# Performance work log

Hardware: AMD Instinct MI355X
Metric: run time of the kernel (lower is better)

## Reference

```python
import jax, jax.numpy as jnp
import numpy as np

NUM_USERS = 50000
NUM_FOODS = 20000
USER_FEAT_DIM = 256
FOOD_FEAT_DIM = 256
EMBED_DIM = 128
NUM_LAYERS = 3
NUM_HEADS = 4
THRESHOLD = 0.3
E_UF = 600000  # user->food interactions; symmetrized to 2*E_UF directed edges


def setup_inputs() -> dict:
    key = jax.random.key(0)
    ks = jax.random.split(key, 12)
    user_feat = jax.random.normal(ks[0], (NUM_USERS, USER_FEAT_DIM), jnp.float32)
    food_feat = jax.random.normal(ks[1], (NUM_FOODS, FOOD_FEAT_DIM), jnp.float32)
    # bipartite edges in global index space, symmetrized (both directions)
    u = jax.random.randint(ks[2], (E_UF,), 0, NUM_USERS)
    f = jax.random.randint(ks[3], (E_UF,), 0, NUM_FOODS) + NUM_USERS
    edge_index = jnp.stack([jnp.concatenate([u, f]), jnp.concatenate([f, u])]).astype(jnp.int64)
    s = 0.02
    W_user = jax.random.normal(ks[4], (USER_FEAT_DIM, EMBED_DIM), jnp.float32) * s
    b_user = jnp.zeros((EMBED_DIM,), jnp.float32)
    W_food = jax.random.normal(ks[5], (FOOD_FEAT_DIM, EMBED_DIM), jnp.float32) * s
    b_food = jnp.zeros((EMBED_DIM,), jnp.float32)
    Wq = jax.random.normal(ks[6], (EMBED_DIM, EMBED_DIM), jnp.float32) * s
    Wk = jax.random.normal(ks[7], (EMBED_DIM, EMBED_DIM), jnp.float32) * s
    channel_weights = jnp.zeros((2,), jnp.float32)  # StructurePooling fusion weights
    user_embed = jax.random.normal(ks[8], (NUM_USERS, EMBED_DIM), jnp.float32) * 0.1
    item_embed = jax.random.normal(ks[9], (NUM_FOODS, EMBED_DIM), jnp.float32) * 0.1
    return {"user_feat": user_feat, "food_feat": food_feat, "edge_index": edge_index,
            "W_user": W_user, "b_user": b_user, "W_food": W_food, "b_food": b_food,
            "Wq": Wq, "Wk": Wk, "channel_weights": channel_weights,
            "user_embed": user_embed, "item_embed": item_embed}


def reference(user_feat, food_feat, edge_index, W_user, b_user, W_food, b_food,
              Wq, Wk, channel_weights, user_embed, item_embed):
    N = NUM_USERS + NUM_FOODS
    Dh = EMBED_DIM // NUM_HEADS
    # feature projections + relu
    user_emb = jax.nn.relu(user_feat @ W_user + b_user)   # [U, D]
    food_emb = jax.nn.relu(food_feat @ W_food + b_food)   # [F, D]
    row, col = edge_index[0], edge_index[1]
    # graph generator: per-edge multi-head cosine similarity between user/food endpoints
    u_idx = jnp.where(row < NUM_USERS, row, col)
    f_idx = jnp.where(row < NUM_USERS, col, row) - NUM_USERS
    q = (user_emb[u_idx] @ Wq).reshape(-1, NUM_HEADS, Dh)  # [E, H, Dh]
    k = (food_emb[f_idx] @ Wk).reshape(-1, NUM_HEADS, Dh)
    eps = 1e-8
    sim = (q * k).sum(-1) / (jnp.linalg.norm(q, axis=-1) * jnp.linalg.norm(k, axis=-1) + eps)
    mask_feature = (sim.mean(-1) > THRESHOLD).astype(jnp.float32)  # [E]
    # structure pooling fusion of [all-ones, feature mask]
    w = jax.nn.softmax(channel_weights)
    fused = w[0] * 1.0 + w[1] * mask_feature
    edge_mask = (fused > 0.5).astype(jnp.float32)
    # LightGCN: symmetric-normalized propagation on the masked graph
    deg = jnp.maximum(jax.ops.segment_sum(edge_mask, row, num_segments=N), 1.0)
    norm = edge_mask / jnp.sqrt(deg[row] * deg[col])       # [E]
    x0 = jnp.concatenate([user_embed, item_embed], axis=0)  # [N, D]
    x = x0
    acc = x0
    for _ in range(NUM_LAYERS):
        x = jax.ops.segment_sum(norm[:, None] * x[col], row, num_segments=N)
        acc = acc + x
    out = acc / float(NUM_LAYERS + 1)
    return (out[:NUM_USERS], out[NUM_USERS:], user_embed, item_embed)
```

## Files before the change

kernel.cpp:

```cpp
#include <hip/hip_runtime.h>
#include <cstdint>

#define U_NUM 50000
#define F_NUM 20000
#define N_NUM 70000
#define D_EMB 128
#define THRESH 0.3f

typedef _Float16 half8 __attribute__((ext_vector_type(8)));
typedef float f32x4 __attribute__((ext_vector_type(4)));
typedef unsigned short u16x8 __attribute__((ext_vector_type(8)));

__global__ void presplit_zero(const float* __restrict__ Wu, const float* __restrict__ Wf,
                              const float* __restrict__ Wq, const float* __restrict__ Wk,
                              unsigned short* __restrict__ dst,
                              int* __restrict__ cnt, int* __restrict__ cursor)
{
    int i = blockIdx.x * 256 + threadIdx.x;
    if (i < N_NUM) { cnt[i] = 0; cursor[i] = 0; }
    if (i >= 98304) return;
    float a; size_t d; int pstride;
    if (i < 32768) {
        int n = i >> 8, k = i & 255;
        a = Wu[k * 128 + n]; d = (size_t)n * 256 + k; pstride = 32768;
    } else if (i < 65536) {
        int j = i - 32768; int n = j >> 8, k = j & 255;
        a = Wf[k * 128 + n]; d = 65536 + (size_t)n * 256 + k; pstride = 32768;
    } else if (i < 81920) {
        int j = i - 65536; int n = j >> 7, k = j & 127;
        a = Wq[k * 128 + n]; d = 131072 + (size_t)n * 128 + k; pstride = 16384;
    } else {
        int j = i - 81920; int n = j >> 7, k = j & 127;
        a = Wk[k * 128 + n]; d = 163840 + (size_t)n * 128 + k; pstride = 16384;
    }
    _Float16 c1 = (_Float16)a;
    float r = a - (float)c1;
    _Float16 c2 = (_Float16)r;
    dst[d]           = __builtin_bit_cast(unsigned short, c1);
    dst[d + pstride] = __builtin_bit_cast(unsigned short, c2);
}

__device__ __forceinline__ void split2(const float4 x0, const float4 x1,
                                       half8& h, half8& lo)
{
    float v[8] = {x0.x, x0.y, x0.z, x0.w, x1.x, x1.y, x1.z, x1.w};
#pragma unroll
    for (int i = 0; i < 8; i++) {
        _Float16 c1 = (_Float16)v[i];
        h[i] = c1;
        lo[i] = (_Float16)(v[i] - (float)c1);
    }
}

__global__ __launch_bounds__(256, 3)
void gemm1(const float* __restrict__ uf, const float* __restrict__ ff,
           const unsigned short* __restrict__ Wsp,
           const float* __restrict__ bu, const float* __restrict__ bfo,
           unsigned short* __restrict__ Eh, int nbU2)
{
    constexpr int NK = 8;
    __shared__ unsigned short Bs[2][2][64][40];

    unsigned short* El = Eh + (size_t)N_NUM * 128;
    const int bid = blockIdx.x;
    const bool isU = bid < nbU2;
    const int lb  = isU ? bid : bid - nbU2;
    const int rowTile = lb >> 1;
    const int n0 = (lb & 1) * 64;
    const int Mloc = isU ? U_NUM : F_NUM;
    const int combBase = isU ? 0 : U_NUM;
    const float* A  = isU ? uf : ff;
    const float* b1 = isU ? bu : bfo;
    const unsigned short* W = Wsp + (isU ? 0 : 65536);
    const int Wp = 32768;

    const int tid = threadIdx.x;
    const int w  = tid >> 6;
    const int l  = tid & 63;
    const int lm = l & 15;
    const int lq = l >> 4;
    const int wr = w * 32;

    const int sp = tid >> 7;
    const int sn = (tid >> 1) & 63;
    const int sh = tid & 1;
    const unsigned short* wsrc = W + (size_t)sp * Wp + (size_t)(n0 + sn) * 256 + sh * 16;

    auto stage = [&](int buf, int kc) {
        const unsigned short* s = wsrc + kc * 32;
        uint4 v0 = *(const uint4*)(s);
        uint4 v1 = *(const uint4*)(s + 8);
        *(uint4*)&Bs[buf][sp][sn][sh * 16]     = v0;
        *(uint4*)&Bs[buf][sp][sn][sh * 16 + 8] = v1;
    };

    const float* arow[2];
#pragma unroll
    for (int rb = 0; rb < 2; ++rb) {
        int r = min(rowTile * 128 + wr + rb * 16 + lm, Mloc - 1);
        arow[rb] = A + (size_t)r * 256 + lq * 8;
    }

    f32x4 acc[2][4];
#pragma unroll
    for (int i = 0; i < 2; i++)
#pragma unroll
        for (int j = 0; j < 4; j++) acc[i][j] = (f32x4)0.f;

    float4 pa0[2], pa1[2];
#pragma unroll
    for (int rb = 0; rb < 2; ++rb) {
        const float4* p4 = (const float4*)(arow[rb]);
        pa0[rb] = p4[0]; pa1[rb] = p4[1];
    }
    stage(0, 0);
    __syncthreads();
    int buf = 0;
#pragma unroll
    for (int kc = 0; kc < NK; ++kc) {
        float4 na0[2], na1[2];
        if (kc + 1 < NK) {
#pragma unroll
            for (int rb = 0; rb < 2; ++rb) {
                const float4* p4 = (const float4*)(arow[rb] + (kc + 1) * 32);
                na0[rb] = p4[0]; na1[rb] = p4[1];
            }
            stage(buf ^ 1, kc + 1);
        }
        half8 a1[2], a2[2];
#pragma unroll
        for (int rb = 0; rb < 2; ++rb) split2(pa0[rb], pa1[rb], a1[rb], a2[rb]);
#pragma unroll
        for (int cb = 0; cb < 4; ++cb) {
            const unsigned short* bp = &Bs[buf][0][cb * 16 + lm][lq * 8];
            half8 bh = *(const half8*)bp;
            half8 bl = *(const half8*)(bp + 64 * 40);
#pragma unroll
            for (int rb = 0; rb < 2; ++rb) {
                acc[rb][cb] = __builtin_amdgcn_mfma_f32_16x16x32_f16(a2[rb], bh, acc[rb][cb], 0, 0, 0);
                acc[rb][cb] = __builtin_amdgcn_mfma_f32_16x16x32_f16(a1[rb], bl, acc[rb][cb], 0, 0, 0);
                acc[rb][cb] = __builtin_amdgcn_mfma_f32_16x16x32_f16(a1[rb], bh, acc[rb][cb], 0, 0, 0);
            }
        }
        __syncthreads();
        if (kc + 1 < NK) {
#pragma unroll
            for (int rb = 0; rb < 2; ++rb) { pa0[rb] = na0[rb]; pa1[rb] = na1[rb]; }
        }
        buf ^= 1;
    }

#pragma unroll
    for (int cb = 0; cb < 4; ++cb) {
        const int col = n0 + cb * 16 + lm;
        const float bb = b1[col];
#pragma unroll
        for (int rb = 0; rb < 2; ++rb)
#pragma unroll
            for (int rg = 0; rg < 4; ++rg) {
                int lr = wr + rb * 16 + lq * 4 + rg;
                if (rowTile * 128 + lr < Mloc) {
                    size_t r = (size_t)(combBase + rowTile * 128 + lr);
                    float e = fmaxf(acc[rb][cb][rg] + bb, 0.f);
                    _Float16 c1 = (_Float16)e;
                    _Float16 c2 = (_Float16)(e - (float)c1);
                    Eh[r * 128 + col] = __builtin_bit_cast(unsigned short, c1);
                    El[r * 128 + col] = __builtin_bit_cast(unsigned short, c2);
                }
            }
    }
}

__global__ __launch_bounds__(256, 3)
void gemm2(const unsigned short* __restrict__ Eh,
           const unsigned short* __restrict__ Wsp,
           float* __restrict__ Qo, unsigned short* __restrict__ QKh, int nbU2)
{
    constexpr int NK = 4;
    __shared__ unsigned short Bs[2][2][64][40];

    const unsigned short* El = Eh + (size_t)N_NUM * 128;
    const int bid = blockIdx.x;
    const bool isU = bid < nbU2;
    const int lb  = isU ? bid : bid - nbU2;
    const int rowTile = lb >> 1;
    const int n0 = (lb & 1) * 64;
    const int Mloc = isU ? U_NUM : F_NUM;
    const int combBase = isU ? 0 : U_NUM;
    const unsigned short* W = Wsp + (isU ? 131072 : 163840);
    const int Wp = 16384;

    const int tid = threadIdx.x;
    const int w  = tid >> 6;
    const int l  = tid & 63;
    const int lm = l & 15;
    const int lq = l >> 4;
    const int wr = w * 32;

    const int sp = tid >> 7;
    const int sn = (tid >> 1) & 63;
    const int sh = tid & 1;
    const unsigned short* wsrc = W + (size_t)sp * Wp + (size_t)(n0 + sn) * 128 + sh * 16;

    auto stage = [&](int buf, int kc) {
        const unsigned short* s = wsrc + kc * 32;
        uint4 v0 = *(const uint4*)(s);
        uint4 v1 = *(const uint4*)(s + 8);
        *(uint4*)&Bs[buf][sp][sn][sh * 16]     = v0;
        *(uint4*)&Bs[buf][sp][sn][sh * 16 + 8] = v1;
    };

    size_t erow[2];
#pragma unroll
    for (int rb = 0; rb < 2; ++rb) {
        int r = min(rowTile * 128 + wr + rb * 16 + lm, Mloc - 1) + combBase;
        erow[rb] = (size_t)r * 128 + lq * 8;
    }

    f32x4 acc[2][4];
#pragma unroll
    for (int i = 0; i < 2; i++)
#pragma unroll
        for (int j = 0; j < 4; j++) acc[i][j] = (f32x4)0.f;

    u16x8 ph[2], pl[2];
#pragma unroll
    for (int rb = 0; rb < 2; ++rb) {
        ph[rb] = *(const u16x8*)(Eh + erow[rb]);
        pl[rb] = *(const u16x8*)(El + erow[rb]);
    }
    stage(0, 0);
    __syncthreads();
    int buf = 0;
#pragma unroll
    for (int kc = 0; kc < NK; ++kc) {
        u16x8 nh[2], nl[2];
        if (kc + 1 < NK) {
#pragma unroll
            for (int rb = 0; rb < 2; ++rb) {
                nh[rb] = *(const u16x8*)(Eh + erow[rb] + (kc + 1) * 32);
                nl[rb] = *(const u16x8*)(El + erow[rb] + (kc + 1) * 32);
            }
            stage(buf ^ 1, kc + 1);
        }
#pragma unroll
        for (int cb = 0; cb < 4; ++cb) {
            const unsigned short* bp = &Bs[buf][0][cb * 16 + lm][lq * 8];
            half8 bh = *(const half8*)bp;
            half8 bl = *(const half8*)(bp + 64 * 40);
#pragma unroll
            for (int rb = 0; rb < 2; ++rb) {
                half8 a1 = __builtin_bit_cast(half8, ph[rb]);
                half8 a2 = __builtin_bit_cast(half8, pl[rb]);
                acc[rb][cb] = __builtin_amdgcn_mfma_f32_16x16x32_f16(a2, bh, acc[rb][cb], 0, 0, 0);
                acc[rb][cb] = __builtin_amdgcn_mfma_f32_16x16x32_f16(a1, bl, acc[rb][cb], 0, 0, 0);
                acc[rb][cb] = __builtin_amdgcn_mfma_f32_16x16x32_f16(a1, bh, acc[rb][cb], 0, 0, 0);
            }
        }
        __syncthreads();
        if (kc + 1 < NK) {
#pragma unroll
            for (int rb = 0; rb < 2; ++rb) { ph[rb] = nh[rb]; pl[rb] = nl[rb]; }
        }
        buf ^= 1;
    }

#pragma unroll
    for (int cb = 0; cb < 4; ++cb) {
        const int col = n0 + cb * 16 + lm;
#pragma unroll
        for (int rb = 0; rb < 2; ++rb)
#pragma unroll
            for (int rg = 0; rg < 4; ++rg) {
                int lr = wr + rb * 16 + lq * 4 + rg;
                if (rowTile * 128 + lr < Mloc) {
                    size_t r = (size_t)(combBase + rowTile * 128 + lr);
                    float v = acc[rb][cb][rg];
                    Qo[r * 128 + col] = v;
                    QKh[r * 128 + col] = __builtin_bit_cast(unsigned short, (_Float16)v);
                }
            }
    }
}

__global__ __launch_bounds__(256)
void edge_kernel(const int* __restrict__ ei, int Edir,
                 const unsigned short* __restrict__ QKh, const float* __restrict__ QKf,
                 const float* __restrict__ cwts,
                 float* __restrict__ maskf, int* __restrict__ cnt, int Eund)
{
    int gid = blockIdx.x * 256 + threadIdx.x;
    int e = gid >> 3;
    if (e >= Eund) return;
    int sub = gid & 7;
    int row = ei[e];
    int col = ei[Edir + e];
    row = min(max(row, 0), N_NUM - 1);
    col = min(max(col, 0), N_NUM - 1);
    int u  = (row < U_NUM) ? row : col;
    int fg = (row < U_NUM) ? col : row;
    u = min(max(u, 0), U_NUM - 1);
    int f = min(max(fg - U_NUM, 0), F_NUM - 1);
    const size_t qrow = (size_t)u * D_EMB;
    const size_t krow = (size_t)(U_NUM + f) * D_EMB;

    const unsigned short* qh = QKh + qrow + sub * 16;
    const unsigned short* kh = QKh + krow + sub * 16;
    u16x8 qa = *(const u16x8*)(qh);
    u16x8 qb = *(const u16x8*)(qh + 8);
    u16x8 ka = *(const u16x8*)(kh);
    u16x8 kb = *(const u16x8*)(kh + 8);
    float dot = 0.f, qq = 0.f, kk = 0.f;
#pragma unroll
    for (int i = 0; i < 8; i++) {
        float qv = (float)__builtin_bit_cast(_Float16, (unsigned short)qa[i]);
        float kv = (float)__builtin_bit_cast(_Float16, (unsigned short)ka[i]);
        dot += qv * kv; qq += qv * qv; kk += kv * kv;
    }
#pragma unroll
    for (int i = 0; i < 8; i++) {
        float qv = (float)__builtin_bit_cast(_Float16, (unsigned short)qb[i]);
        float kv = (float)__builtin_bit_cast(_Float16, (unsigned short)kb[i]);
        dot += qv * kv; qq += qv * qv; kk += kv * kv;
    }
    dot += __shfl_xor(dot, 1);
    qq  += __shfl_xor(qq, 1);
    kk  += __shfl_xor(kk, 1);
    float denom = sqrtf(qq) * sqrtf(kk) + 1e-8f;
    float sim = dot / denom;
    float s = sim + __shfl_xor(sim, 2);
    s += __shfl_xor(s, 4);
    float mean = s * 0.25f;

    if (fabsf(mean - THRESH) < 0.03f) {
        const float4* qp = (const float4*)(QKf + qrow + sub * 16);
        const float4* kp = (const float4*)(QKf + krow + sub * 16);
        float dot2 = 0.f, qq2 = 0.f, kk2 = 0.f;
#pragma unroll
        for (int i = 0; i < 4; i++) {
            float4 a = qp[i]; float4 b = kp[i];
            dot2 += a.x * b.x + a.y * b.y + a.z * b.z + a.w * b.w;
            qq2  += a.x * a.x + a.y * a.y + a.z * a.z + a.w * a.w;
            kk2  += b.x * b.x + b.y * b.y + b.z * b.z + b.w * b.w;
        }
        dot2 += __shfl_xor(dot2, 1);
        qq2  += __shfl_xor(qq2, 1);
        kk2  += __shfl_xor(kk2, 1);
        float denom2 = sqrtf(qq2) * sqrtf(kk2) + 1e-8f;
        float sim2 = dot2 / denom2;
        float s2 = sim2 + __shfl_xor(sim2, 2);
        s2 += __shfl_xor(s2, 4);
        mean = s2 * 0.25f;
    }

    float mf = (mean > THRESH) ? 1.f : 0.f;
    float cw0 = cwts[0], cw1 = cwts[1];
    float mx = fmaxf(cw0, cw1);
    float e0 = expf(cw0 - mx), e1 = expf(cw1 - mx);
    float inv = 1.f / (e0 + e1);
    float fused = e0 * inv + (e1 * inv) * mf;
    float em = (fused > 0.5f) ? 1.f : 0.f;

    if (sub == 0) {
        maskf[e] = em;
        if (em != 0.f) {
            atomicAdd(&cnt[row], 1);
            atomicAdd(&cnt[col], 1);
        }
    }
}

__global__ void scan_part(const int* __restrict__ cnt, int* __restrict__ part, int n)
{
    __shared__ int sd[256];
    int b = blockIdx.x, t = threadIdx.x;
    int base = b * 1024;
    int s = 0;
#pragma unroll
    for (int j = 0; j < 4; j++) {
        int idx = base + t + j * 256;
        if (idx < n) s += cnt[idx];
    }
    sd[t] = s; __syncthreads();
    for (int d = 128; d > 0; d >>= 1) {
        if (t < d) sd[t] += sd[t + d];
        __syncthreads();
    }
    if (t == 0) part[b] = sd[0];
}

__global__ void scan_small(int* part, int nb)
{
    __shared__ int sd[256];
    int t = threadIdx.x;
    sd[t] = (t < nb) ? part[t] : 0;
    __syncthreads();
    for (int d = 1; d < 256; d <<= 1) {
        int x = (t >= d) ? sd[t - d] : 0;
        __syncthreads();
        sd[t] += x;
        __syncthreads();
    }
    if (t < nb) part[t] = (t > 0) ? sd[t - 1] : 0;
}

__global__ void scan_final(const int* __restrict__ cnt, const int* __restrict__ part,
                           int* __restrict__ offs, int n)
{
    __shared__ int sd[256];
    int b = blockIdx.x, t = threadIdx.x;
    int base = b * 1024 + t * 4;
    int v[4]; int s = 0;
#pragma unroll
    for (int j = 0; j < 4; j++) {
        int idx = base + j;
        v[j] = (idx < n) ? cnt[idx] : 0;
        s += v[j];
    }
    sd[t] = s; __syncthreads();
    for (int d = 1; d < 256; d <<= 1) {
        int x = (t >= d) ? sd[t - d] : 0;
        __syncthreads();
        sd[t] += x;
        __syncthreads();
    }
    int prefix = part[b] + ((t > 0) ? sd[t - 1] : 0);
#pragma unroll
    for (int j = 0; j < 4; j++) {
        int idx = base + j;
        if (idx < n) offs[idx] = prefix;
        prefix += v[j];
    }
}

__global__ void scatter_kernel(const int* __restrict__ ei, int Edir,
                               const float* __restrict__ maskf,
                               const int* __restrict__ cnt, const int* __restrict__ offs,
                               int* __restrict__ cursor,
                               int* __restrict__ cnbr, float* __restrict__ cwA, int Eund)
{
    int e = blockIdx.x * 256 + threadIdx.x;
    if (e >= Eund) return;
    if (maskf[e] == 0.f) return;
    int row = ei[e], col = ei[Edir + e];
    row = min(max(row, 0), N_NUM - 1);
    col = min(max(col, 0), N_NUM - 1);
    float w = 1.0f / sqrtf((float)cnt[row] * (float)cnt[col]);
    int p1 = offs[row] + atomicAdd(&cursor[row], 1);
    cnbr[p1] = col; cwA[p1] = w;
    int p2 = offs[col] + atomicAdd(&cursor[col], 1);
    cnbr[p2] = row; cwA[p2] = w;
}

template<int MODE>
__global__ __launch_bounds__(256)
void prop(const int* __restrict__ offs, const int* __restrict__ cnt,
          const int* __restrict__ cnbr, const float* __restrict__ cwA,
          const float* __restrict__ xin,
          const float* __restrict__ ue, const float* __restrict__ ie,
          const float* __restrict__ x1b, float* __restrict__ xout,
          float* __restrict__ tail)
{
    int wid = (blockIdx.x << 2) + (threadIdx.x >> 6);
    if (wid >= N_NUM) return;
    int lane = threadIdx.x & 63;
    int num = cnt[wid];
    if (MODE != 2 && num == 0) return;
    int start = (num > 0) ? offs[wid] : 0;
    float ax = 0.f, ay = 0.f;

    auto srcp = [&](int c) -> const float* {
        if (MODE == 0)
            return (c < U_NUM) ? (ue + (size_t)c * D_EMB) : (ie + (size_t)(c - U_NUM) * D_EMB);
        else
            return xin + (size_t)c * D_EMB;
    };

    int j = 0;
    for (; j + 4 <= num; j += 4) {
        int c0i = cnbr[start + j],     c1i = cnbr[start + j + 1];
        int c2i = cnbr[start + j + 2], c3i = cnbr[start + j + 3];
        float w0 = cwA[start + j],     w1 = cwA[start + j + 1];
        float w2 = cwA[start + j + 2], w3 = cwA[start + j + 3];
        float2 v0 = *(const float2*)(srcp(c0i) + lane * 2);
        float2 v1 = *(const float2*)(srcp(c1i) + lane * 2);
        float2 v2 = *(const float2*)(srcp(c2i) + lane * 2);
        float2 v3 = *(const float2*)(srcp(c3i) + lane * 2);
        ax += w0 * v0.x; ay += w0 * v0.y;
        ax += w1 * v1.x; ay += w1 * v1.y;
        ax += w2 * v2.x; ay += w2 * v2.y;
        ax += w3 * v3.x; ay += w3 * v3.y;
    }
    for (; j < num; ++j) {
        int c = cnbr[start + j]; float w = cwA[start + j];
        float2 v = *(const float2*)(srcp(c) + lane * 2);
        ax += w * v.x; ay += w * v.y;
    }

    size_t o = (size_t)wid * D_EMB + lane * 2;
    if (MODE == 2) {
        const float* x0p = (wid < U_NUM) ? (ue + (size_t)wid * D_EMB)
                                         : (ie + (size_t)(wid - U_NUM) * D_EMB);
        float2 x0v = *(const float2*)(x0p + lane * 2);
        *(float2*)(tail + o) = x0v;
        float ox, oy;
        if (num == 0) {
            ox = x0v.x * 0.25f; oy = x0v.y * 0.25f;
        } else {
            float2 x1v = *(const float2*)(x1b + o);
            float2 x2v = *(const float2*)(xin + o);
            ox = ((x0v.x + x1v.x) + x2v.x + ax) * 0.25f;
            oy = ((x0v.y + x1v.y) + x2v.y + ay) * 0.25f;
        }
        *(float2*)(xout + o) = make_float2(ox, oy);
    } else {
        *(float2*)(xout + o) = make_float2(ax, ay);
    }
}

extern "C" void kernel_launch(void* const* d_in, const int* in_sizes, int n_in,
                              void* d_out, int out_size, void* d_ws, size_t ws_size,
                              hipStream_t stream)
{
    const float* user_feat  = (const float*)d_in[0];
    const float* food_feat  = (const float*)d_in[1];
    const int*   ei         = (const int*)d_in[2];
    const float* W_user     = (const float*)d_in[3];
    const float* b_user     = (const float*)d_in[4];
    const float* W_food     = (const float*)d_in[5];
    const float* b_food     = (const float*)d_in[6];
    const float* Wq         = (const float*)d_in[7];
    const float* Wk         = (const float*)d_in[8];
    const float* cwts       = (const float*)d_in[9];
    const float* user_embed = (const float*)d_in[10];
    const float* item_embed = (const float*)d_in[11];

    const int Edir = in_sizes[2] / 2;
    const int Eund = Edir / 2;

    char* ws = (char*)d_ws;
    size_t off = 0;
    auto alloc = [&](size_t nb) { size_t o = off; off += (nb + 255) & ~(size_t)255; return o; };

    float* Q     = (float*)(ws + alloc((size_t)N_NUM * D_EMB * 4));
    float* xB    = (float*)(ws + alloc((size_t)N_NUM * D_EMB * 4));
    unsigned short* QKh = (unsigned short*)(ws + alloc((size_t)N_NUM * D_EMB * 2));
    float* maskf = (float*)(ws + alloc((size_t)Eund * 4));
    int*   cnt   = (int*)  (ws + alloc((size_t)N_NUM * 4));
    int*   offs  = (int*)  (ws + alloc((size_t)N_NUM * 4));
    int*   cursor= (int*)  (ws + alloc((size_t)N_NUM * 4));
    int*   cnbr  = (int*)  (ws + alloc((size_t)Edir * 4));
    float* cwA   = (float*)(ws + alloc((size_t)Edir * 4));
    int*   part  = (int*)  (ws + alloc((size_t)256 * 4));
    unsigned short* Wsp = (unsigned short*)(ws + alloc((size_t)196608 * 2));
    (void)ws_size; (void)n_in; (void)out_size;

    float* xA = Q;
    unsigned short* Ehl = (unsigned short*)xB;

    presplit_zero<<<384, 256, 0, stream>>>(W_user, W_food, Wq, Wk, Wsp, cnt, cursor);

    const int nbU2 = 2 * ((U_NUM + 127) / 128);
    const int nbF2 = 2 * ((F_NUM + 127) / 128);
    gemm1<<<nbU2 + nbF2, 256, 0, stream>>>(user_feat, food_feat, Wsp, b_user, b_food,
                                           Ehl, nbU2);
    gemm2<<<nbU2 + nbF2, 256, 0, stream>>>(Ehl, Wsp, Q, QKh, nbU2);

    edge_kernel<<<(Eund * 8 + 255) / 256, 256, 0, stream>>>(ei, Edir, QKh, Q, cwts,
                                                            maskf, cnt, Eund);

    int nb = (N_NUM + 1023) / 1024;
    scan_part <<<nb, 256, 0, stream>>>(cnt, part, N_NUM);
    scan_small<<<1, 256, 0, stream>>>(part, nb);
    scan_final<<<nb, 256, 0, stream>>>(cnt, part, offs, N_NUM);

    scatter_kernel<<<(Eund + 255) / 256, 256, 0, stream>>>(ei, Edir, maskf, cnt, offs,
                                                           cursor, cnbr, cwA, Eund);

    int pb = (N_NUM + 3) / 4;
    float* tail = (float*)d_out + (size_t)N_NUM * D_EMB;
    prop<0><<<pb, 256, 0, stream>>>(offs, cnt, cnbr, cwA, nullptr, user_embed, item_embed,
                                    nullptr, xB, nullptr);
    prop<1><<<pb, 256, 0, stream>>>(offs, cnt, cnbr, cwA, xB, user_embed, item_embed,
                                    nullptr, xA, nullptr);
    prop<2><<<pb, 256, 0, stream>>>(offs, cnt, cnbr, cwA, xA, user_embed, item_embed,
                                    xB, (float*)d_out, tail);
}
```

Baseline: 161.3 us.

## Preload full weight slabs into LDS and narrow gemm1 column tiles

Both projection GEMMs now load their whole split-fp16 weight slab into shared memory once, before the K loop. This removes the per-iteration double-buffered staging and the barrier on every K step. gemm1 also drops from 64-column to 32-column tiles, so it launches twice as many blocks, and both kernels raise the occupancy hint to 4 blocks per CU. The cost is that gemm1 reads each fp32 A row four times instead of twice, and gemm2 needs a larger LDS footprint.

```diff
diff --git a/kernel.cpp b/kernel.cpp
--- a/kernel.cpp
+++ b/kernel.cpp
@@ -52,48 +52,50 @@
     }
 }
 
-__global__ __launch_bounds__(256, 3)
+__global__ __launch_bounds__(256, 4)
 void gemm1(const float* __restrict__ uf, const float* __restrict__ ff,
            const unsigned short* __restrict__ Wsp,
            const float* __restrict__ bu, const float* __restrict__ bfo,
-           unsigned short* __restrict__ Eh, int nbU2)
-{
-    constexpr int NK = 8;
-    __shared__ unsigned short Bs[2][2][64][40];
+           unsigned short* __restrict__ Eh, int nbU4)
+{
+    __shared__ unsigned short Ws[2][8][32][40];
 
     unsigned short* El = Eh + (size_t)N_NUM * 128;
     const int bid = blockIdx.x;
-    const bool isU = bid < nbU2;
-    const int lb  = isU ? bid : bid - nbU2;
-    const int rowTile = lb >> 1;
-    const int n0 = (lb & 1) * 64;
+    const bool isU = bid < nbU4;
+    const int lb  = isU ? bid : bid - nbU4;
+    const int rowTile = lb >> 2;
+    const int n0 = (lb & 3) * 32;
     const int Mloc = isU ? U_NUM : F_NUM;
     const int combBase = isU ? 0 : U_NUM;
     const float* A  = isU ? uf : ff;
     const float* b1 = isU ? bu : bfo;
     const unsigned short* W = Wsp + (isU ? 0 : 65536);
-    const int Wp = 32768;
 
     const int tid = threadIdx.x;
+
+    {
+        int pn = tid >> 2, q = tid & 3;
+        int p = pn >> 5, n = pn & 31;
+        const unsigned short* src = W + (size_t)p * 32768 + (size_t)(n0 + n) * 256 + q * 64;
+#pragma unroll
+        for (int c = 0; c < 2; ++c) {
+            uint4 v0 = *(const uint4*)(src + c * 32);
+            uint4 v1 = *(const uint4*)(src + c * 32 + 8);
+            uint4 v2 = *(const uint4*)(src + c * 32 + 16);
+            uint4 v3 = *(const uint4*)(src + c * 32 + 24);
+            unsigned short* d = &Ws[p][q * 2 + c][n][0];
+            ((uint4*)d)[0] = v0; ((uint4*)d)[1] = v1;
+            ((uint4*)d)[2] = v2; ((uint4*)d)[3] = v3;
+        }
+    }
+
     const int w  = tid >> 6;
     const int l  = tid & 63;
     const int lm = l & 15;
     const int lq = l >> 4;
     const int wr = w * 32;
 
-    const int sp = tid >> 7;
-    const int sn = (tid >> 1) & 63;
-    const int sh = tid & 1;
-    const unsigned short* wsrc = W + (size_t)sp * Wp + (size_t)(n0 + sn) * 256 + sh * 16;
-
-    auto stage = [&](int buf, int kc) {
-        const unsigned short* s = wsrc + kc * 32;
-        uint4 v0 = *(const uint4*)(s);
-        uint4 v1 = *(const uint4*)(s + 8);
-        *(uint4*)&Bs[buf][sp][sn][sh * 16]     = v0;
-        *(uint4*)&Bs[buf][sp][sn][sh * 16 + 8] = v1;
-    };
-
     const float* arow[2];
 #pragma unroll
     for (int rb = 0; rb < 2; ++rb) {
@@ -101,11 +103,13 @@
         arow[rb] = A + (size_t)r * 256 + lq * 8;
     }
 
-    f32x4 acc[2][4];
+    __syncthreads();
+
+    f32x4 acc[2][2];
 #pragma unroll
     for (int i = 0; i < 2; i++)
 #pragma unroll
-        for (int j = 0; j < 4; j++) acc[i][j] = (f32x4)0.f;
+        for (int j = 0; j < 2; j++) acc[i][j] = (f32x4)0.f;
 
     float4 pa0[2], pa1[2];
 #pragma unroll
@@ -113,28 +117,23 @@
         const float4* p4 = (const float4*)(arow[rb]);
         pa0[rb] = p4[0]; pa1[rb] = p4[1];
     }
-    stage(0, 0);
-    __syncthreads();
-    int buf = 0;
-#pragma unroll
-    for (int kc = 0; kc < NK; ++kc) {
+#pragma unroll
+    for (int kc = 0; kc < 8; ++kc) {
         float4 na0[2], na1[2];
-        if (kc + 1 < NK) {
+        if (kc < 7) {
 #pragma unroll
             for (int rb = 0; rb < 2; ++rb) {
                 const float4* p4 = (const float4*)(arow[rb] + (kc + 1) * 32);
                 na0[rb] = p4[0]; na1[rb] = p4[1];
             }
-            stage(buf ^ 1, kc + 1);
         }
         half8 a1[2], a2[2];
 #pragma unroll
         for (int rb = 0; rb < 2; ++rb) split2(pa0[rb], pa1[rb], a1[rb], a2[rb]);
 #pragma unroll
-        for (int cb = 0; cb < 4; ++cb) {
-            const unsigned short* bp = &Bs[buf][0][cb * 16 + lm][lq * 8];
-            half8 bh = *(const half8*)bp;
-            half8 bl = *(const half8*)(bp + 64 * 40);
+        for (int cb = 0; cb < 2; ++cb) {
+            half8 bh = *(const half8*)&Ws[0][kc][cb * 16 + lm][lq * 8];
+            half8 bl = *(const half8*)&Ws[1][kc][cb * 16 + lm][lq * 8];
 #pragma unroll
             for (int rb = 0; rb < 2; ++rb) {
                 acc[rb][cb] = __builtin_amdgcn_mfma_f32_16x16x32_f16(a2[rb], bh, acc[rb][cb], 0, 0, 0);
@@ -142,16 +141,14 @@
                 acc[rb][cb] = __builtin_amdgcn_mfma_f32_16x16x32_f16(a1[rb], bh, acc[rb][cb], 0, 0, 0);
             }
         }
-        __syncthreads();
-        if (kc + 1 < NK) {
+        if (kc < 7) {
 #pragma unroll
             for (int rb = 0; rb < 2; ++rb) { pa0[rb] = na0[rb]; pa1[rb] = na1[rb]; }
         }
-        buf ^= 1;
-    }
-
-#pragma unroll
-    for (int cb = 0; cb < 4; ++cb) {
+    }
+
+#pragma unroll
+    for (int cb = 0; cb < 2; ++cb) {
         const int col = n0 + cb * 16 + lm;
         const float bb = b1[col];
 #pragma unroll
@@ -171,13 +168,12 @@
     }
 }
 
-__global__ __launch_bounds__(256, 3)
+__global__ __launch_bounds__(256, 4)
 void gemm2(const unsigned short* __restrict__ Eh,
            const unsigned short* __restrict__ Wsp,
            float* __restrict__ Qo, unsigned short* __restrict__ QKh, int nbU2)
 {
-    constexpr int NK = 4;
-    __shared__ unsigned short Bs[2][2][64][40];
+    __shared__ unsigned short Ws[2][4][64][40];
 
     const unsigned short* El = Eh + (size_t)N_NUM * 128;
     const int bid = blockIdx.x;
@@ -188,28 +184,31 @@
     const int Mloc = isU ? U_NUM : F_NUM;
     const int combBase = isU ? 0 : U_NUM;
     const unsigned short* W = Wsp + (isU ? 131072 : 163840);
-    const int Wp = 16384;
 
     const int tid = threadIdx.x;
+
+    {
+        int pn = tid >> 1, h = tid & 1;
+        int p = pn >> 6, n = pn & 63;
+        const unsigned short* src = W + (size_t)p * 16384 + (size_t)(n0 + n) * 128 + h * 64;
+#pragma unroll
+        for (int c = 0; c < 2; ++c) {
+            uint4 v0 = *(const uint4*)(src + c * 32);
+            uint4 v1 = *(const uint4*)(src + c * 32 + 8);
+            uint4 v2 = *(const uint4*)(src + c * 32 + 16);
+            uint4 v3 = *(const uint4*)(src + c * 32 + 24);
+            unsigned short* d = &Ws[p][h * 2 + c][n][0];
+            ((uint4*)d)[0] = v0; ((uint4*)d)[1] = v1;
+            ((uint4*)d)[2] = v2; ((uint4*)d)[3] = v3;
+        }
+    }
+
     const int w  = tid >> 6;
     const int l  = tid & 63;
     const int lm = l & 15;
     const int lq = l >> 4;
     const int wr = w * 32;
 
-    const int sp = tid >> 7;
-    const int sn = (tid >> 1) & 63;
-    const int sh = tid & 1;
-    const unsigned short* wsrc = W + (size_t)sp * Wp + (size_t)(n0 + sn) * 128 + sh * 16;
-
-    auto stage = [&](int buf, int kc) {
-        const unsigned short* s = wsrc + kc * 32;
-        uint4 v0 = *(const uint4*)(s);
-        uint4 v1 = *(const uint4*)(s + 8);
-        *(uint4*)&Bs[buf][sp][sn][sh * 16]     = v0;
-        *(uint4*)&Bs[buf][sp][sn][sh * 16 + 8] = v1;
-    };
-
     size_t erow[2];
 #pragma unroll
     for (int rb = 0; rb < 2; ++rb) {
@@ -217,6 +216,8 @@
         erow[rb] = (size_t)r * 128 + lq * 8;
     }
 
+    __syncthreads();
+
     f32x4 acc[2][4];
 #pragma unroll
     for (int i = 0; i < 2; i++)
@@ -229,25 +230,20 @@
         ph[rb] = *(const u16x8*)(Eh + erow[rb]);
         pl[rb] = *(const u16x8*)(El + erow[rb]);
     }
-    stage(0, 0);
-    __syncthreads();
-    int buf = 0;
-#pragma unroll
-    for (int kc = 0; kc < NK; ++kc) {
+#pragma unroll
+    for (int kc = 0; kc < 4; ++kc) {
         u16x8 nh[2], nl[2];
-        if (kc + 1 < NK) {
+        if (kc < 3) {
 #pragma unroll
             for (int rb = 0; rb < 2; ++rb) {
                 nh[rb] = *(const u16x8*)(Eh + erow[rb] + (kc + 1) * 32);
                 nl[rb] = *(const u16x8*)(El + erow[rb] + (kc + 1) * 32);
             }
-            stage(buf ^ 1, kc + 1);
         }
 #pragma unroll
         for (int cb = 0; cb < 4; ++cb) {
-            const unsigned short* bp = &Bs[buf][0][cb * 16 + lm][lq * 8];
-            half8 bh = *(const half8*)bp;
-            half8 bl = *(const half8*)(bp + 64 * 40);
+            half8 bh = *(const half8*)&Ws[0][kc][cb * 16 + lm][lq * 8];
+            half8 bl = *(const half8*)&Ws[1][kc][cb * 16 + lm][lq * 8];
 #pragma unroll
             for (int rb = 0; rb < 2; ++rb) {
                 half8 a1 = __builtin_bit_cast(half8, ph[rb]);
@@ -257,12 +253,10 @@
                 acc[rb][cb] = __builtin_amdgcn_mfma_f32_16x16x32_f16(a1, bh, acc[rb][cb], 0, 0, 0);
             }
         }
-        __syncthreads();
-        if (kc + 1 < NK) {
+        if (kc < 3) {
 #pragma unroll
             for (int rb = 0; rb < 2; ++rb) { ph[rb] = nh[rb]; pl[rb] = nl[rb]; }
         }
-        buf ^= 1;
     }
 
 #pragma unroll
@@ -560,10 +554,12 @@
 
     presplit_zero<<<384, 256, 0, stream>>>(W_user, W_food, Wq, Wk, Wsp, cnt, cursor);
 
+    const int nbU4 = 4 * ((U_NUM + 127) / 128);
+    const int nbF4 = 4 * ((F_NUM + 127) / 128);
+    gemm1<<<nbU4 + nbF4, 256, 0, stream>>>(user_feat, food_feat, Wsp, b_user, b_food,
+                                           Ehl, nbU4);
     const int nbU2 = 2 * ((U_NUM + 127) / 128);
     const int nbF2 = 2 * ((F_NUM + 127) / 128);
-    gemm1<<<nbU2 + nbF2, 256, 0, stream>>>(user_feat, food_feat, Wsp, b_user, b_food,
-                                           Ehl, nbU2);
     gemm2<<<nbU2 + nbF2, 256, 0, stream>>>(Ehl, Wsp, Q, QKh, nbU2);
 
     edge_kernel<<<(Eund * 8 + 255) / 256, 256, 0, stream>>>(ei, Edir, QKh, Q, cwts,
```

After: 181.2 us. +12.4%, slower.
